# Kernel optimization log

Hardware: AMD Instinct MI355X
Metric: run time of the kernel (lower is better)

Reference implementation:

```python
import jax, jax.numpy as jnp
import numpy as np

B, T, D = 8, 1024, 1024
H, HS = 16, 64  # num_heads, head_size; H*HS == D


def setup_inputs() -> dict:
    key = jax.random.key(0)
    ks = jax.random.split(key, 5)
    scale = 0.02
    x = jax.random.normal(ks[0], (B, T, D), dtype=jnp.float32)
    Wq = jax.random.normal(ks[1], (H, D, HS), dtype=jnp.float32) * scale
    Wk = jax.random.normal(ks[2], (H, D, HS), dtype=jnp.float32) * scale
    Wv = jax.random.normal(ks[3], (H, D, HS), dtype=jnp.float32) * scale
    Wo = jax.random.normal(ks[4], (D, D), dtype=jnp.float32) * scale
    bo = jnp.zeros((D,), dtype=jnp.float32)
    return {"x": x, "Wq": Wq, "Wk": Wk, "Wv": Wv, "Wo": Wo, "bo": bo}


def reference(x, Wq, Wk, Wv, Wo, bo):
    # Per-head linear projections (bias-free, as in Head): [B,H,T,HS]
    q = jnp.einsum('btd,hds->bhts', x, Wq)
    k = jnp.einsum('btd,hds->bhts', x, Wk)
    v = jnp.einsum('btd,hds->bhts', x, Wv)
    # Scaled scores with causal mask: [B,H,T,T]
    scores = jnp.einsum('bhts,bhus->bhtu', q, k) * (HS ** -0.5)
    causal = jnp.tril(jnp.ones((T, T), dtype=bool))
    scores = jnp.where(causal, scores, jnp.finfo(scores.dtype).min)
    att = jax.nn.softmax(scores, axis=-1)
    # Weighted sum over values, then concat heads: [B,T,H*HS]
    out = jnp.einsum('bhtu,bhus->bhts', att, v)
    out = out.transpose(0, 2, 1, 3).reshape(B, T, H * HS)
    # Output projection (nn.Linear: y = x @ W^T + b)
    return out @ Wo.T + bo
```

## Files before the change

### kernel.cpp

```cpp
#include <hip/hip_runtime.h>
#include <hip/hip_bf16.h>

#define BBATCH 8
#define TSEQ   1024
#define DMODEL 1024
#define NHEAD  16
#define HSZ    64

typedef unsigned short ushort_t;
typedef __attribute__((ext_vector_type(8))) short short8;
typedef __attribute__((ext_vector_type(4))) float float4v;

__device__ __forceinline__ ushort_t f2bf(float f) {
    __hip_bfloat16 h = __float2bfloat16(f);
    return *reinterpret_cast<ushort_t*>(&h);
}
__device__ __forceinline__ ushort_t f2bf_fast(float f) {
    return (ushort_t)((__float_as_uint(f) + 0x8000u) >> 16);
}
__device__ __forceinline__ unsigned int pack_bf2(float lo, float hi) {
    unsigned int a = __float_as_uint(lo) + 0x8000u;
    unsigned int b = __float_as_uint(hi) + 0x8000u;
    return __builtin_amdgcn_perm(b, a, 0x07060302u);
}

__device__ __forceinline__ short8 cvt8(const float* f) {
    union { ushort_t u[8]; short8 v; } r;
    #pragma unroll
    for (int e = 0; e < 8; ++e) r.u[e] = f2bf(f[e]);
    return r.v;
}

__device__ __forceinline__ void async16(const ushort_t* g, ushort_t* l) {
    __builtin_amdgcn_global_load_lds(
        (const __attribute__((address_space(1))) unsigned int*)g,
        (__attribute__((address_space(3))) unsigned int*)l, 16, 0, 0);
}

__global__ __launch_bounds__(256) void cvt_f32_bf16(
    const float* __restrict__ src, ushort_t* __restrict__ dst)
{
    const size_t idx = ((size_t)blockIdx.x * 256 + threadIdx.x) * 16;
    float f[16];
    *(float4*)(f + 0)  = *(const float4*)(src + idx);
    *(float4*)(f + 4)  = *(const float4*)(src + idx + 4);
    *(float4*)(f + 8)  = *(const float4*)(src + idx + 8);
    *(float4*)(f + 12) = *(const float4*)(src + idx + 12);
    uint4 o0 = make_uint4(pack_bf2(f[0], f[1]),   pack_bf2(f[2], f[3]),
                          pack_bf2(f[4], f[5]),   pack_bf2(f[6], f[7]));
    uint4 o1 = make_uint4(pack_bf2(f[8], f[9]),   pack_bf2(f[10], f[11]),
                          pack_bf2(f[12], f[13]), pack_bf2(f[14], f[15]));
    *(uint4*)(dst + idx) = o0;
    *(uint4*)(dst + idx + 8) = o1;
}

__global__ __launch_bounds__(256) void pack_w(
    const float* __restrict__ Wq, const float* __restrict__ Wk,
    const float* __restrict__ Wv, ushort_t* __restrict__ WpT)
{
    __shared__ ushort_t L[64 * 72];
    const int tid = threadIdx.x;
    const int d0 = blockIdx.x * 64;
    const int wh = blockIdx.y;
    const int w = wh >> 4, h = wh & 15;
    const float* W = (w == 0 ? Wq : (w == 1 ? Wk : Wv)) + (size_t)h * DMODEL * HSZ;

    int dr = tid >> 2, sc = (tid & 3) * 16;
    const float4* src = (const float4*)(W + (size_t)(d0 + dr) * HSZ + sc);
    float f[16];
    *(float4*)(f + 0) = src[0]; *(float4*)(f + 4) = src[1];
    *(float4*)(f + 8) = src[2]; *(float4*)(f + 12) = src[3];
    *(short8*)(L + dr * 72 + sc)     = cvt8(f);
    *(short8*)(L + dr * 72 + sc + 8) = cvt8(f + 8);
    __syncthreads();

    int s = tid >> 2, dc = (tid & 3) * 16;
    union { ushort_t u[16]; short8 v[2]; } o;
    #pragma unroll
    for (int j = 0; j < 16; ++j) o.u[j] = L[(dc + j) * 72 + s];
    ushort_t* dst = WpT + (size_t)(w * 1024 + h * 64 + s) * DMODEL + d0 + dc;
    *(short8*)dst = o.v[0];
    *(short8*)(dst + 8) = o.v[1];
}

template<bool STG, int VW>
__device__ __forceinline__ void ktile_step(
    ushort_t* As, ushort_t* Bs,
    const ushort_t* (&gA)[4], const ushort_t* (&gB)[4],
    const int wave,
    const int aoff0, const int aoff1, const int boff0, const int boff1,
    float4v (&acc)[8][4])
{
    short8 avA[4][2], avB[4][2], bv[2][2];

    #pragma unroll
    for (int a = 0; a < 4; ++a) {
        avA[a][0] = *(const short8*)(As + aoff0 + a * 1024);
        avA[a][1] = *(const short8*)(As + aoff1 + a * 1024);
    }
    #pragma unroll
    for (int b = 0; b < 2; ++b) {
        bv[b][0] = *(const short8*)(Bs + boff0 + b * 1024);
        bv[b][1] = *(const short8*)(Bs + boff1 + b * 1024);
    }
    __builtin_amdgcn_s_barrier();
    __builtin_amdgcn_s_setprio(1);
    #pragma unroll
    for (int kth = 0; kth < 2; ++kth)
        #pragma unroll
        for (int a = 0; a < 4; ++a)
            #pragma unroll
            for (int b = 0; b < 2; ++b)
                acc[a][b] = __builtin_amdgcn_mfma_f32_16x16x32_bf16(
                    avA[a][kth], bv[b][kth], acc[a][b], 0, 0, 0);
    __builtin_amdgcn_s_setprio(0);
    __builtin_amdgcn_s_barrier();

    #pragma unroll
    for (int a = 0; a < 4; ++a) {
        avB[a][0] = *(const short8*)(As + aoff0 + (a + 4) * 1024);
        avB[a][1] = *(const short8*)(As + aoff1 + (a + 4) * 1024);
    }
    __builtin_amdgcn_s_barrier();
    __builtin_amdgcn_s_setprio(1);
    #pragma unroll
    for (int kth = 0; kth < 2; ++kth)
        #pragma unroll
        for (int a = 0; a < 4; ++a)
            #pragma unroll
            for (int b = 0; b < 2; ++b)
                acc[a + 4][b] = __builtin_amdgcn_mfma_f32_16x16x32_bf16(
                    avB[a][kth], bv[b][kth], acc[a + 4][b], 0, 0, 0);
    __builtin_amdgcn_s_setprio(0);
    __builtin_amdgcn_s_barrier();

    #pragma unroll
    for (int b = 0; b < 2; ++b) {
        bv[b][0] = *(const short8*)(Bs + boff0 + (b + 2) * 1024);
        bv[b][1] = *(const short8*)(Bs + boff1 + (b + 2) * 1024);
    }
    __builtin_amdgcn_s_barrier();
    __builtin_amdgcn_s_setprio(1);
    #pragma unroll
    for (int kth = 0; kth < 2; ++kth)
        #pragma unroll
        for (int a = 0; a < 4; ++a)
            #pragma unroll
            for (int b = 0; b < 2; ++b)
                acc[a][b + 2] = __builtin_amdgcn_mfma_f32_16x16x32_bf16(
                    avA[a][kth], bv[b][kth], acc[a][b + 2], 0, 0, 0);
    __builtin_amdgcn_s_setprio(0);
    __builtin_amdgcn_s_barrier();

    if (STG) {
        #pragma unroll
        for (int i = 0; i < 4; ++i) {
            async16(gA[i], As + i * 4096 + wave * 512);
            async16(gB[i], Bs + i * 4096 + wave * 512);
            gA[i] += 64; gB[i] += 64;
        }
    }
    __builtin_amdgcn_s_barrier();
    __builtin_amdgcn_s_setprio(1);
    #pragma unroll
    for (int kth = 0; kth < 2; ++kth)
        #pragma unroll
        for (int a = 0; a < 4; ++a)
            #pragma unroll
            for (int b = 0; b < 2; ++b)
                acc[a + 4][b + 2] = __builtin_amdgcn_mfma_f32_16x16x32_bf16(
                    avB[a][kth], bv[b][kth], acc[a + 4][b + 2], 0, 0, 0);
    __builtin_amdgcn_s_setprio(0);
    if (VW == 8)      asm volatile("s_waitcnt vmcnt(8)" ::: "memory");
    else if (VW == 0) asm volatile("s_waitcnt vmcnt(0)" ::: "memory");
    __builtin_amdgcn_s_barrier();
}

__global__ __launch_bounds__(512, 2) void qkv_gemm(
    const ushort_t* __restrict__ Xb, const ushort_t* __restrict__ WpT,
    ushort_t* __restrict__ Qb, ushort_t* __restrict__ Kb, ushort_t* __restrict__ Vt)
{
    __shared__ ushort_t As0[256 * 64];
    __shared__ ushort_t Bs0[256 * 64];
    __shared__ ushort_t As1[256 * 64];
    __shared__ ushort_t Bs1[256 * 64];

    const int tid = threadIdx.x;
    const int wave = tid >> 6, lane = tid & 63;
    const int q = lane >> 4, cc = lane & 15;
    const int wm = wave >> 2, wn = wave & 3;

    const int bid = blockIdx.x;
    const int xcd = bid & 7, lo = bid >> 3;
    const bool isV = (lo >= 32);
    int tn, tm;
    if (!isV) { tn = lo >> 2;        tm = xcd * 4 + (lo & 3); }
    else      { int v = lo - 32; tn = v >> 2; tm = xcd * 4 + (v & 3); }
    const int n0 = (isV ? 2048 : 0) + tn * 256;
    const int m0 = tm * 256;

    const ushort_t* pA = isV ? Xb + (size_t)m0 * DMODEL : WpT + (size_t)n0 * DMODEL;
    const ushort_t* pB = isV ? WpT + (size_t)n0 * DMODEL : Xb + (size_t)m0 * DMODEL;

    const int srow = lane >> 3;
    const int chx = (lane & 7) ^ srow;
    const ushort_t* gA[4]; const ushort_t* gB[4];
    #pragma unroll
    for (int i = 0; i < 4; ++i) {
        int row = i * 64 + wave * 8 + srow;
        gA[i] = pA + (size_t)row * DMODEL + chx * 8;
        gB[i] = pB + (size_t)row * DMODEL + chx * 8;
    }

    const int c7 = cc & 7;
    const int arow = wm * 128 + cc;
    const int brow = wn * 64 + cc;
    const int aoff0 = arow * 64 + ((q ^ c7) * 8);
    const int aoff1 = arow * 64 + (((4 + q) ^ c7) * 8);
    const int boff0 = brow * 64 + ((q ^ c7) * 8);
    const int boff1 = brow * 64 + (((4 + q) ^ c7) * 8);

    float4v acc[8][4];
    #pragma unroll
    for (int a = 0; a < 8; ++a)
        #pragma unroll
        for (int b = 0; b < 4; ++b) acc[a][b] = (float4v){0.f, 0.f, 0.f, 0.f};

    #pragma unroll
    for (int i = 0; i < 4; ++i) {
        async16(gA[i], As0 + i * 4096 + wave * 512);
        async16(gB[i], Bs0 + i * 4096 + wave * 512);
        gA[i] += 64; gB[i] += 64;
    }
    #pragma unroll
    for (int i = 0; i < 4; ++i) {
        async16(gA[i], As1 + i * 4096 + wave * 512);
        async16(gB[i], Bs1 + i * 4096 + wave * 512);
        gA[i] += 64; gB[i] += 64;
    }
    asm volatile("s_waitcnt vmcnt(8)" ::: "memory");
    __builtin_amdgcn_s_barrier();

    #pragma unroll 1
    for (int it = 0; it < 7; ++it) {
        ktile_step<true, 8>(As0, Bs0, gA, gB, wave, aoff0, aoff1, boff0, boff1, acc);
        ktile_step<true, 8>(As1, Bs1, gA, gB, wave, aoff0, aoff1, boff0, boff1, acc);
    }
    ktile_step<false, 0>(As0, Bs0, gA, gB, wave, aoff0, aoff1, boff0, boff1, acc);
    ktile_step<false, -1>(As1, Bs1, gA, gB, wave, aoff0, aoff1, boff0, boff1, acc);

    if (!isV) {
        ushort_t* Out = (n0 < 1024) ? Qb : Kb;
        const float osc = (n0 < 1024) ? 0.18033688011112042f : 1.0f;
        #pragma unroll
        for (int a = 0; a < 8; ++a) {
            int nr = n0 + wm * 128 + a * 16 + q * 4;
            int h = (nr >> 6) & 15, s0 = nr & 63;
            #pragma unroll
            for (int b = 0; b < 4; ++b) {
                int mc = m0 + wn * 64 + b * 16 + cc;
                int bb = mc >> 10, t = mc & 1023;
                size_t addr = (((size_t)(bb * NHEAD + h)) * TSEQ + t) * HSZ + s0;
                uint2 pk = make_uint2(
                    pack_bf2(acc[a][b][0] * osc, acc[a][b][1] * osc),
                    pack_bf2(acc[a][b][2] * osc, acc[a][b][3] * osc));
                *(uint2*)(Out + addr) = pk;
            }
        }
    } else {
        #pragma unroll
        for (int a = 0; a < 8; ++a) {
            int mr = m0 + wm * 128 + a * 16 + q * 4;
            int bb = mr >> 10, t0 = mr & 1023;
            #pragma unroll
            for (int b = 0; b < 4; ++b) {
                int nc = n0 + wn * 64 + b * 16 + cc;
                int h = (nc >> 6) & 15, s = nc & 63;
                size_t addr = (((size_t)(bb * NHEAD + h)) * HSZ + s) * TSEQ + t0;
                uint2 pk = make_uint2(pack_bf2(acc[a][b][0], acc[a][b][1]),
                                      pack_bf2(acc[a][b][2], acc[a][b][3]));
                *(uint2*)(Vt + addr) = pk;
            }
        }
    }
}

__global__ __launch_bounds__(256) void attn(
    const ushort_t* __restrict__ Qb, const ushort_t* __restrict__ Kb,
    const ushort_t* __restrict__ Vt, ushort_t* __restrict__ Ob)
{
    __shared__ ushort_t Ks[2][64 * 64];
    __shared__ ushort_t VTs[2][64 * 64];
    __shared__ ushort_t Ps[4][32 * 72];
    const int tid = threadIdx.x;
    const int wave = tid >> 6, lane = tid & 63;
    const int q = lane >> 4, cc = lane & 15;
    const int bid = blockIdx.x;
    const int qt = 7 - (bid >> 7);
    const int bh = bid & 127;
    const size_t base = (size_t)bh * TSEQ * HSZ;
    const int J = 2 * qt + 2;

    const ushort_t* kg[2]; const ushort_t* vg[2]; int dmo[2];
    #pragma unroll
    for (int i = 0; i < 2; ++i) {
        int rr = wave * 16 + i * 8 + (lane >> 3);
        int ch = (lane & 7) ^ (rr & 7);
        kg[i] = Kb + base + (size_t)rr * HSZ + ch * 8;
        vg[i] = Vt + base + (size_t)rr * TSEQ + ch * 8;
        dmo[i] = (wave * 16 + i * 8) * 64;
    }

    short8 qf[2][2];
    #pragma unroll
    for (int tt = 0; tt < 2; ++tt) {
        const ushort_t* qp = Qb + base +
            (size_t)(qt * 128 + wave * 32 + tt * 16 + cc) * HSZ + q * 8;
        qf[tt][0] = *(const short8*)qp;
        qf[tt][1] = *(const short8*)(qp + 32);
    }

    int koff[4][2], poff[2][2];
    #pragma unroll
    for (int ut = 0; ut < 4; ++ut)
        #pragma unroll
        for (int kt = 0; kt < 2; ++kt)
            koff[ut][kt] = (ut * 16 + cc) * 64 + (((kt * 4 + q) ^ (cc & 7)) * 8);
    #pragma unroll
    for (int tt = 0; tt < 2; ++tt)
        #pragma unroll
        for (int kt = 0; kt < 2; ++kt)
            poff[tt][kt] = (tt * 16 + cc) * 72 + kt * 32 + q * 8;

    float4v oacc[2][4];
    #pragma unroll
    for (int tt = 0; tt < 2; ++tt)
        #pragma unroll
        for (int st = 0; st < 4; ++st) oacc[tt][st] = (float4v){0.f, 0.f, 0.f, 0.f};
    float lsum[2] = {0.f, 0.f};

    #pragma unroll
    for (int i = 0; i < 2; ++i) {
        async16(kg[i], &Ks[0][dmo[i]]);
        async16(vg[i], &VTs[0][dmo[i]]);
    }
    __syncthreads();

    for (int jt = 0; jt < J; ++jt) {
        const ushort_t* Kc = Ks[jt & 1];
        const ushort_t* Vc = VTs[jt & 1];
        if (jt + 1 < J) {
            int nb = (jt + 1) & 1;
            #pragma unroll
            for (int i = 0; i < 2; ++i) {
                async16(kg[i] + (size_t)(jt + 1) * 64 * HSZ, &Ks[nb][dmo[i]]);
                async16(vg[i] + (jt + 1) * 64, &VTs[nb][dmo[i]]);
            }
        }

        float4v sc[4][2];
        #pragma unroll
        for (int ut = 0; ut < 4; ++ut)
            #pragma unroll
            for (int tt = 0; tt < 2; ++tt) sc[ut][tt] = (float4v){0.f, 0.f, 0.f, 0.f};
        #pragma unroll
        for (int kt = 0; kt < 2; ++kt) {
            short8 kf[4];
            #pragma unroll
            for (int ut = 0; ut < 4; ++ut) kf[ut] = *(const short8*)(Kc + koff[ut][kt]);
            #pragma unroll
            for (int ut = 0; ut < 4; ++ut) {
                sc[ut][0] = __builtin_amdgcn_mfma_f32_16x16x32_bf16(
                    kf[ut], qf[0][kt], sc[ut][0], 0, 0, 0);
                sc[ut][1] = __builtin_amdgcn_mfma_f32_16x16x32_bf16(
                    kf[ut], qf[1][kt], sc[ut][1], 0, 0, 0);
            }
        }

        if ((jt >> 1) == qt) {
            #pragma unroll
            for (int tt = 0; tt < 2; ++tt) {
                const int tg = qt * 128 + wave * 32 + tt * 16 + cc;
                #pragma unroll
                for (int ut = 0; ut < 4; ++ut) {
                    float pv[4]; float ps = 0.f;
                    #pragma unroll
                    for (int rr = 0; rr < 4; ++rr) {
                        float p = exp2f(sc[ut][tt][rr]);
                        if ((jt * 64 + ut * 16 + q * 4 + rr) > tg) p = 0.f;
                        pv[rr] = p; ps += p;
                    }
                    lsum[tt] += ps;
                    *(uint2*)&Ps[wave][(tt * 16 + cc) * 72 + ut * 16 + q * 4] =
                        make_uint2(pack_bf2(pv[0], pv[1]), pack_bf2(pv[2], pv[3]));
                }
            }
        } else {
            #pragma unroll
            for (int tt = 0; tt < 2; ++tt) {
                #pragma unroll
                for (int ut = 0; ut < 4; ++ut) {
                    float pv[4]; float ps = 0.f;
                    #pragma unroll
                    for (int rr = 0; rr < 4; ++rr) {
                        float p = exp2f(sc[ut][tt][rr]);
                        pv[rr] = p; ps += p;
                    }
                    lsum[tt] += ps;
                    *(uint2*)&Ps[wave][(tt * 16 + cc) * 72 + ut * 16 + q * 4] =
                        make_uint2(pack_bf2(pv[0], pv[1]), pack_bf2(pv[2], pv[3]));
                }
            }
        }

        #pragma unroll
        for (int kt = 0; kt < 2; ++kt) {
            short8 pa0 = *(const short8*)&Ps[wave][poff[0][kt]];
            short8 pa1 = *(const short8*)&Ps[wave][poff[1][kt]];
            #pragma unroll
            for (int st = 0; st < 4; ++st) {
                short8 vf = *(const short8*)(Vc + koff[st][kt]);
                oacc[0][st] = __builtin_amdgcn_mfma_f32_16x16x32_bf16(
                    pa0, vf, oacc[0][st], 0, 0, 0);
                oacc[1][st] = __builtin_amdgcn_mfma_f32_16x16x32_bf16(
                    pa1, vf, oacc[1][st], 0, 0, 0);
            }
        }
        __syncthreads();
    }

    float inv[2];
    #pragma unroll
    for (int tt = 0; tt < 2; ++tt) {
        float l = lsum[tt];
        l += __shfl_xor(l, 16);
        l += __shfl_xor(l, 32);
        inv[tt] = 1.f / l;
    }
    const int b = bh >> 4, h = bh & 15;
    #pragma unroll
    for (int tt = 0; tt < 2; ++tt)
        #pragma unroll
        for (int rr = 0; rr < 4; ++rr) {
            float iv = __shfl(inv[tt], q * 4 + rr);
            int t = qt * 128 + wave * 32 + tt * 16 + q * 4 + rr;
            size_t rb = ((size_t)b * TSEQ + t) * DMODEL + h * HSZ;
            #pragma unroll
            for (int st = 0; st < 4; ++st)
                Ob[rb + st * 16 + cc] = f2bf_fast(oacc[tt][st][rr] * iv);
        }
}

__global__ __launch_bounds__(256) void oproj_gemm(
    const ushort_t* __restrict__ Obuf, const ushort_t* __restrict__ Wob,
    const float* __restrict__ bo, float* __restrict__ out)
{
    __shared__ ushort_t As[128 * 64];
    __shared__ ushort_t Bs[128 * 64];
    const int tid = threadIdx.x;
    const int wave = tid >> 6, lane = tid & 63;
    const int q = lane >> 4, cc = lane & 15;
    const int bid = blockIdx.x;
    const int xcd = bid & 7, local = bid >> 3;
    const int n0 = (local >> 3) * 128;
    const int m0 = (xcd * 8 + (local & 7)) * 128;
    const int wm = wave >> 1, wn = wave & 1;

    const ushort_t* ag[4]; const ushort_t* bg[4]; int lo_[4];
    #pragma unroll
    for (int i = 0; i < 4; ++i) {
        int row = wave * 32 + i * 8 + (lane >> 3);
        int ch = (lane & 7) ^ (row & 7);
        ag[i] = Obuf + (size_t)(m0 + row) * DMODEL + ch * 8;
        bg[i] = Wob + (size_t)(n0 + row) * DMODEL + ch * 8;
        lo_[i] = (wave * 32 + i * 8) * 64;
    }
    int aoff[4][2], boff[4][2];
    #pragma unroll
    for (int mt = 0; mt < 4; ++mt) {
        int row = wm * 64 + mt * 16 + cc;
        #pragma unroll
        for (int kt = 0; kt < 2; ++kt)
            aoff[mt][kt] = row * 64 + (((kt * 4 + q) ^ (row & 7)) * 8);
    }
    #pragma unroll
    for (int nt = 0; nt < 4; ++nt) {
        int row = wn * 64 + nt * 16 + cc;
        #pragma unroll
        for (int kt = 0; kt < 2; ++kt)
            boff[nt][kt] = row * 64 + (((kt * 4 + q) ^ (row & 7)) * 8);
    }

    float4v acc[4][4];
    #pragma unroll
    for (int a = 0; a < 4; ++a)
        #pragma unroll
        for (int b = 0; b < 4; ++b) acc[a][b] = (float4v){0.f, 0.f, 0.f, 0.f};

    for (int j = 0; j < 16; ++j) {
        #pragma unroll
        for (int i = 0; i < 4; ++i) {
            async16(ag[i], As + lo_[i]);
            async16(bg[i], Bs + lo_[i]);
            ag[i] += 64; bg[i] += 64;
        }
        __syncthreads();

        short8 av[4][2], bv[4][2];
        #pragma unroll
        for (int mt = 0; mt < 4; ++mt) {
            av[mt][0] = *(const short8*)(As + aoff[mt][0]);
            av[mt][1] = *(const short8*)(As + aoff[mt][1]);
        }
        #pragma unroll
        for (int nt = 0; nt < 4; ++nt) {
            bv[nt][0] = *(const short8*)(Bs + boff[nt][0]);
            bv[nt][1] = *(const short8*)(Bs + boff[nt][1]);
        }
        #pragma unroll
        for (int kt = 0; kt < 2; ++kt)
            #pragma unroll
            for (int mt = 0; mt < 4; ++mt)
                #pragma unroll
                for (int nt = 0; nt < 4; ++nt)
                    acc[mt][nt] = __builtin_amdgcn_mfma_f32_16x16x32_bf16(
                        av[mt][kt], bv[nt][kt], acc[mt][nt], 0, 0, 0);
        __syncthreads();
    }

    #pragma unroll
    for (int nt = 0; nt < 4; ++nt) {
        int n = n0 + wn * 64 + nt * 16 + cc;
        float bias = bo[n];
        #pragma unroll
        for (int mt = 0; mt < 4; ++mt)
            #pragma unroll
            for (int rr = 0; rr < 4; ++rr) {
                int m = m0 + wm * 64 + mt * 16 + q * 4 + rr;
                out[(size_t)m * DMODEL + n] = acc[mt][nt][rr] + bias;
            }
    }
}

extern "C" void kernel_launch(void* const* d_in, const int* in_sizes, int n_in,
                              void* d_out, int out_size, void* d_ws, size_t ws_size,
                              hipStream_t stream)
{
    const float* x  = (const float*)d_in[0];
    const float* Wq = (const float*)d_in[1];
    const float* Wk = (const float*)d_in[2];
    const float* Wv = (const float*)d_in[3];
    const float* Wo = (const float*)d_in[4];
    const float* bo = (const float*)d_in[5];
    float* out = (float*)d_out;

    const size_t SEG = (size_t)8 * 1024 * 1024;
    ushort_t* Qb  = (ushort_t*)d_ws;
    ushort_t* Kb  = Qb + SEG;
    ushort_t* Vtb = Kb + SEG;
    ushort_t* WpT = Vtb + SEG;
    ushort_t* Ob  = WpT;
    ushort_t* Xb  = (ushort_t*)d_out;
    ushort_t* Wob = Qb;

    cvt_f32_bf16<<<dim3(2048),    256, 0, stream>>>(x, Xb);
    pack_w      <<<dim3(16, 48),  256, 0, stream>>>(Wq, Wk, Wv, WpT);
    qkv_gemm    <<<dim3(384),     512, 0, stream>>>(Xb, WpT, Qb, Kb, Vtb);
    attn        <<<dim3(1024),    256, 0, stream>>>(Qb, Kb, Vtb, Ob);
    cvt_f32_bf16<<<dim3(256),     256, 0, stream>>>(Wo, Wob);
    oproj_gemm  <<<dim3(512),     256, 0, stream>>>(Ob, Wob, bo, out);
}
```

Baseline: 253.9 us.

## Interleave next-tile async loads across MFMA phases in QKV GEMM pipeline

Restructures the QKV GEMM double-buffer pipeline. Loads for the next k-tile are now issued into the other buffer in pairs across the four MFMA phases, with finer vmcnt waits, and only one tile is prefetched in the prologue. The MFMA phase order is changed so the loaded A/B fragments are reused in a snake order, and the epilogue store loops are swapped. The aim is to spread global-to-LDS traffic over the step and shorten prologue latency, at the cost of a shallower prefetch distance that could expose memory latency.

Result: faster. 237.1 us (-6.6%).

```diff
diff --git a/kernel.cpp b/kernel.cpp
--- a/kernel.cpp
+++ b/kernel.cpp
@@ -35,6 +35,12 @@
     __builtin_amdgcn_global_load_lds(
         (const __attribute__((address_space(1))) unsigned int*)g,
         (__attribute__((address_space(3))) unsigned int*)l, 16, 0, 0);
+}
+
+template<int N> __device__ __forceinline__ void vwait() {
+    if constexpr (N == 4)      asm volatile("s_waitcnt vmcnt(4)" ::: "memory");
+    else if constexpr (N == 2) asm volatile("s_waitcnt vmcnt(2)" ::: "memory");
+    else if constexpr (N == 0) asm volatile("s_waitcnt vmcnt(0)" ::: "memory");
 }
 
 __global__ __launch_bounds__(256) void cvt_f32_bf16(
@@ -83,96 +89,108 @@
     *(short8*)(dst + 8) = o.v[1];
 }
 
-template<bool STG, int VW>
+template<bool STG, int W0, int W1, int W3>
 __device__ __forceinline__ void ktile_step(
     ushort_t* As, ushort_t* Bs,
+    ushort_t* An, ushort_t* Bn,
     const ushort_t* (&gA)[4], const ushort_t* (&gB)[4],
     const int wave,
     const int aoff0, const int aoff1, const int boff0, const int boff1,
     float4v (&acc)[8][4])
 {
-    short8 avA[4][2], avB[4][2], bv[2][2];
+    short8 aLo[4][2], aHi[4][2], bLo[2][2], bHi[2][2];
 
     #pragma unroll
     for (int a = 0; a < 4; ++a) {
-        avA[a][0] = *(const short8*)(As + aoff0 + a * 1024);
-        avA[a][1] = *(const short8*)(As + aoff1 + a * 1024);
+        aLo[a][0] = *(const short8*)(As + aoff0 + a * 1024);
+        aLo[a][1] = *(const short8*)(As + aoff1 + a * 1024);
     }
     #pragma unroll
     for (int b = 0; b < 2; ++b) {
-        bv[b][0] = *(const short8*)(Bs + boff0 + b * 1024);
-        bv[b][1] = *(const short8*)(Bs + boff1 + b * 1024);
+        bLo[b][0] = *(const short8*)(Bs + boff0 + b * 1024);
+        bLo[b][1] = *(const short8*)(Bs + boff1 + b * 1024);
+    }
+    if (STG) {
+        async16(gA[0], An + 0 * 4096 + wave * 512);
+        async16(gA[1], An + 1 * 4096 + wave * 512);
     }
     __builtin_amdgcn_s_barrier();
     __builtin_amdgcn_s_setprio(1);
     #pragma unroll
-    for (int kth = 0; kth < 2; ++kth)
+    for (int k = 0; k < 2; ++k)
         #pragma unroll
         for (int a = 0; a < 4; ++a)
             #pragma unroll
             for (int b = 0; b < 2; ++b)
                 acc[a][b] = __builtin_amdgcn_mfma_f32_16x16x32_bf16(
-                    avA[a][kth], bv[b][kth], acc[a][b], 0, 0, 0);
+                    aLo[a][k], bLo[b][k], acc[a][b], 0, 0, 0);
     __builtin_amdgcn_s_setprio(0);
+    vwait<W0>();
     __builtin_amdgcn_s_barrier();
 
     #pragma unroll
     for (int a = 0; a < 4; ++a) {
-        avB[a][0] = *(const short8*)(As + aoff0 + (a + 4) * 1024);
-        avB[a][1] = *(const short8*)(As + aoff1 + (a + 4) * 1024);
+        aHi[a][0] = *(const short8*)(As + aoff0 + (a + 4) * 1024);
+        aHi[a][1] = *(const short8*)(As + aoff1 + (a + 4) * 1024);
+    }
+    if (STG) {
+        async16(gB[0], Bn + 0 * 4096 + wave * 512);
+        async16(gB[1], Bn + 1 * 4096 + wave * 512);
     }
     __builtin_amdgcn_s_barrier();
     __builtin_amdgcn_s_setprio(1);
     #pragma unroll
-    for (int kth = 0; kth < 2; ++kth)
+    for (int k = 0; k < 2; ++k)
         #pragma unroll
         for (int a = 0; a < 4; ++a)
             #pragma unroll
             for (int b = 0; b < 2; ++b)
                 acc[a + 4][b] = __builtin_amdgcn_mfma_f32_16x16x32_bf16(
-                    avB[a][kth], bv[b][kth], acc[a + 4][b], 0, 0, 0);
+                    aHi[a][k], bLo[b][k], acc[a + 4][b], 0, 0, 0);
     __builtin_amdgcn_s_setprio(0);
+    vwait<W1>();
     __builtin_amdgcn_s_barrier();
 
     #pragma unroll
     for (int b = 0; b < 2; ++b) {
-        bv[b][0] = *(const short8*)(Bs + boff0 + (b + 2) * 1024);
-        bv[b][1] = *(const short8*)(Bs + boff1 + (b + 2) * 1024);
+        bHi[b][0] = *(const short8*)(Bs + boff0 + (b + 2) * 1024);
+        bHi[b][1] = *(const short8*)(Bs + boff1 + (b + 2) * 1024);
+    }
+    if (STG) {
+        async16(gA[2], An + 2 * 4096 + wave * 512);
+        async16(gA[3], An + 3 * 4096 + wave * 512);
     }
     __builtin_amdgcn_s_barrier();
     __builtin_amdgcn_s_setprio(1);
     #pragma unroll
-    for (int kth = 0; kth < 2; ++kth)
+    for (int k = 0; k < 2; ++k)
+        #pragma unroll
+        for (int a = 0; a < 4; ++a)
+            #pragma unroll
+            for (int b = 0; b < 2; ++b)
+                acc[a + 4][b + 2] = __builtin_amdgcn_mfma_f32_16x16x32_bf16(
+                    aHi[a][k], bHi[b][k], acc[a + 4][b + 2], 0, 0, 0);
+    __builtin_amdgcn_s_setprio(0);
+    __builtin_amdgcn_s_barrier();
+
+    if (STG) {
+        async16(gB[2], Bn + 2 * 4096 + wave * 512);
+        async16(gB[3], Bn + 3 * 4096 + wave * 512);
+        #pragma unroll
+        for (int i = 0; i < 4; ++i) { gA[i] += 64; gB[i] += 64; }
+    }
+    __builtin_amdgcn_s_barrier();
+    __builtin_amdgcn_s_setprio(1);
+    #pragma unroll
+    for (int k = 0; k < 2; ++k)
         #pragma unroll
         for (int a = 0; a < 4; ++a)
             #pragma unroll
             for (int b = 0; b < 2; ++b)
                 acc[a][b + 2] = __builtin_amdgcn_mfma_f32_16x16x32_bf16(
-                    avA[a][kth], bv[b][kth], acc[a][b + 2], 0, 0, 0);
+                    aLo[a][k], bHi[b][k], acc[a][b + 2], 0, 0, 0);
     __builtin_amdgcn_s_setprio(0);
-    __builtin_amdgcn_s_barrier();
-
-    if (STG) {
-        #pragma unroll
-        for (int i = 0; i < 4; ++i) {
-            async16(gA[i], As + i * 4096 + wave * 512);
-            async16(gB[i], Bs + i * 4096 + wave * 512);
-            gA[i] += 64; gB[i] += 64;
-        }
-    }
-    __builtin_amdgcn_s_barrier();
-    __builtin_amdgcn_s_setprio(1);
-    #pragma unroll
-    for (int kth = 0; kth < 2; ++kth)
-        #pragma unroll
-        for (int a = 0; a < 4; ++a)
-            #pragma unroll
-            for (int b = 0; b < 2; ++b)
-                acc[a + 4][b + 2] = __builtin_amdgcn_mfma_f32_16x16x32_bf16(
-                    avB[a][kth], bv[b][kth], acc[a + 4][b + 2], 0, 0, 0);
-    __builtin_amdgcn_s_setprio(0);
-    if (VW == 8)      asm volatile("s_waitcnt vmcnt(8)" ::: "memory");
-    else if (VW == 0) asm volatile("s_waitcnt vmcnt(0)" ::: "memory");
+    vwait<W3>();
     __builtin_amdgcn_s_barrier();
 }
 
@@ -226,40 +244,42 @@
         #pragma unroll
         for (int b = 0; b < 4; ++b) acc[a][b] = (float4v){0.f, 0.f, 0.f, 0.f};
 
-    #pragma unroll
-    for (int i = 0; i < 4; ++i) {
-        async16(gA[i], As0 + i * 4096 + wave * 512);
-        async16(gB[i], Bs0 + i * 4096 + wave * 512);
-        gA[i] += 64; gB[i] += 64;
-    }
-    #pragma unroll
-    for (int i = 0; i < 4; ++i) {
-        async16(gA[i], As1 + i * 4096 + wave * 512);
-        async16(gB[i], Bs1 + i * 4096 + wave * 512);
-        gA[i] += 64; gB[i] += 64;
-    }
-    asm volatile("s_waitcnt vmcnt(8)" ::: "memory");
+    async16(gA[0], As0 + 0 * 4096 + wave * 512);
+    async16(gA[1], As0 + 1 * 4096 + wave * 512);
+    async16(gB[0], Bs0 + 0 * 4096 + wave * 512);
+    async16(gB[1], Bs0 + 1 * 4096 + wave * 512);
+    async16(gA[2], As0 + 2 * 4096 + wave * 512);
+    async16(gA[3], As0 + 3 * 4096 + wave * 512);
+    async16(gB[2], Bs0 + 2 * 4096 + wave * 512);
+    async16(gB[3], Bs0 + 3 * 4096 + wave * 512);
+    #pragma unroll
+    for (int i = 0; i < 4; ++i) { gA[i] += 64; gB[i] += 64; }
+    asm volatile("s_waitcnt vmcnt(0)" ::: "memory");
     __builtin_amdgcn_s_barrier();
 
     #pragma unroll 1
     for (int it = 0; it < 7; ++it) {
-        ktile_step<true, 8>(As0, Bs0, gA, gB, wave, aoff0, aoff1, boff0, boff1, acc);
-        ktile_step<true, 8>(As1, Bs1, gA, gB, wave, aoff0, aoff1, boff0, boff1, acc);
-    }
-    ktile_step<false, 0>(As0, Bs0, gA, gB, wave, aoff0, aoff1, boff0, boff1, acc);
-    ktile_step<false, -1>(As1, Bs1, gA, gB, wave, aoff0, aoff1, boff0, boff1, acc);
+        ktile_step<true, 4, 4, 4>(As0, Bs0, As1, Bs1, gA, gB, wave,
+                                  aoff0, aoff1, boff0, boff1, acc);
+        ktile_step<true, 4, 4, 4>(As1, Bs1, As0, Bs0, gA, gB, wave,
+                                  aoff0, aoff1, boff0, boff1, acc);
+    }
+    ktile_step<true, 4, 4, 4>(As0, Bs0, As1, Bs1, gA, gB, wave,
+                              aoff0, aoff1, boff0, boff1, acc);
+    ktile_step<false, 2, 0, -1>(As1, Bs1, As0, Bs0, gA, gB, wave,
+                                aoff0, aoff1, boff0, boff1, acc);
 
     if (!isV) {
         ushort_t* Out = (n0 < 1024) ? Qb : Kb;
         const float osc = (n0 < 1024) ? 0.18033688011112042f : 1.0f;
         #pragma unroll
-        for (int a = 0; a < 8; ++a) {
-            int nr = n0 + wm * 128 + a * 16 + q * 4;
-            int h = (nr >> 6) & 15, s0 = nr & 63;
-            #pragma unroll
-            for (int b = 0; b < 4; ++b) {
-                int mc = m0 + wn * 64 + b * 16 + cc;
-                int bb = mc >> 10, t = mc & 1023;
+        for (int b = 0; b < 4; ++b) {
+            int mc = m0 + wn * 64 + b * 16 + cc;
+            int bb = mc >> 10, t = mc & 1023;
+            #pragma unroll
+            for (int a = 0; a < 8; ++a) {
+                int nr = n0 + wm * 128 + a * 16 + q * 4;
+                int h = (nr >> 6) & 15, s0 = nr & 63;
                 size_t addr = (((size_t)(bb * NHEAD + h)) * TSEQ + t) * HSZ + s0;
                 uint2 pk = make_uint2(
                     pack_bf2(acc[a][b][0] * osc, acc[a][b][1] * osc),
@@ -269,13 +289,13 @@
         }
     } else {
         #pragma unroll
-        for (int a = 0; a < 8; ++a) {
-            int mr = m0 + wm * 128 + a * 16 + q * 4;
-            int bb = mr >> 10, t0 = mr & 1023;
-            #pragma unroll
-            for (int b = 0; b < 4; ++b) {
-                int nc = n0 + wn * 64 + b * 16 + cc;
-                int h = (nc >> 6) & 15, s = nc & 63;
+        for (int b = 0; b < 4; ++b) {
+            int nc = n0 + wn * 64 + b * 16 + cc;
+            int h = (nc >> 6) & 15, s = nc & 63;
+            #pragma unroll
+            for (int a = 0; a < 8; ++a) {
+                int mr = m0 + wm * 128 + a * 16 + q * 4;
+                int bb = mr >> 10, t0 = mr & 1023;
                 size_t addr = (((size_t)(bb * NHEAD + h)) * HSZ + s) * TSEQ + t0;
                 uint2 pk = make_uint2(pack_bf2(acc[a][b][0], acc[a][b][1]),
                                       pack_bf2(acc[a][b][2], acc[a][b][3]));
```
